# Kernel optimization log

Measured on AMD Instinct MI355X. Metric: run time of the kernel, lower is better.

The kernel has to match this reference:

```python
import jax, jax.numpy as jnp
import numpy as np

N_ANCHORS = 10647
N_CLASSES = 80
N_OUT = 5 + N_CLASSES
N_GT = 2048
POS_IOU = 0.7
NEG_IOU = 0.3
N_SAMPLE = 256
POS_RATIO = 0.5


def _cxcy_to_corners(b):
    return jnp.concatenate([b[:, :2] - b[:, 2:4] / 2, b[:, :2] + b[:, 2:4] / 2], axis=-1)


def _iou(a, b):
    # a: [N,4] corner boxes, b: [M,4] corner boxes -> [N,M]
    lt = jnp.maximum(a[:, None, :2], b[None, :, :2])
    rb = jnp.minimum(a[:, None, 2:], b[None, :, 2:])
    wh = jnp.clip(rb - lt, 0.0)
    inter = wh[..., 0] * wh[..., 1]
    area_a = (a[:, 2] - a[:, 0]) * (a[:, 3] - a[:, 1])
    area_b = (b[:, 2] - b[:, 0]) * (b[:, 3] - b[:, 1])
    return inter / (area_a[:, None] + area_b[None, :] - inter)


def _bce_logits(x, t):
    # numerically stable BCEWithLogits, elementwise
    return jnp.maximum(x, 0.0) - x * t + jnp.log1p(jnp.exp(-jnp.abs(x)))


def _demote_first(labels, value, excess):
    # demote the first `excess` anchors (in index order) whose label == value to -1,
    # mirroring torch's nonzero()[randperm(excess)] which always hits the first
    # `excess` entries of the nonzero list
    m = labels == value
    cum = jnp.cumsum(m.astype(jnp.int32))
    return jnp.where(m & (cum <= excess), -1.0, labels)


def _generate_targets(priors, gt_boxes, gt_labels):
    ious = _iou(_cxcy_to_corners(priors[:, :4]), _cxcy_to_corners(gt_boxes))  # [N, M]
    gt_max_index = jnp.argmax(ious, axis=0)       # [M] best anchor per gt
    anchor_max_ious = jnp.max(ious, axis=1)       # [N]
    anchor_max_index = jnp.argmax(ious, axis=1)   # [N]
    labels = jnp.full((N_ANCHORS,), -1.0, dtype=ious.dtype)
    labels = labels.at[gt_max_index].set(1.0)
    labels = jnp.where(anchor_max_ious >= POS_IOU, 1.0, labels)
    labels = jnp.where(anchor_max_ious < NEG_IOU, 0.0, labels)
    n_pos_quota = int(POS_RATIO * N_SAMPLE)
    n_pos_actual = jnp.sum(labels == 1.0)
    labels = _demote_first(labels, 1.0, jnp.maximum(n_pos_actual - n_pos_quota, 0))
    n_neg_req = N_SAMPLE - jnp.sum(labels == 1.0)
    n_neg_actual = jnp.sum(labels == 0.0)
    labels = _demote_first(labels, 0.0, jnp.maximum(n_neg_actual - n_neg_req, 0))
    anchor_gt_box = gt_boxes[anchor_max_index]    # [N,4] matched gt box per anchor
    anchor_cls = gt_labels[anchor_max_index] + 5  # [N] one-hot class column per anchor
    targets = jnp.zeros((N_ANCHORS, N_OUT), dtype=gt_boxes.dtype)
    targets = targets.at[:, :4].set(anchor_gt_box)
    targets = targets.at[:, 4].set(labels)
    targets = targets.at[jnp.arange(N_ANCHORS), anchor_cls].set(1.0)
    return targets


def _forward(predictions, gt_boxes, gt_labels, priors):
    targets = _generate_targets(priors, gt_boxes, gt_labels)
    pred = predictions[0]                          # [N, N_OUT]
    labels = targets[:, 4]
    pos = (labels == 1.0).astype(pred.dtype)
    neg = (labels == 0.0).astype(pred.dtype)
    n_pos = jnp.maximum(jnp.sum(pos), 1.0)
    n_neg = jnp.maximum(jnp.sum(neg), 1.0)
    # masked-mean MSE over x,y,w,h on positive anchors
    diff2 = (pred[:, :4] - targets[:, :4]) ** 2
    loss_box = jnp.sum(pos[:, None] * diff2, axis=0) / n_pos
    loss_conf_obj = jnp.sum(pos * _bce_logits(pred[:, 4], targets[:, 4])) / n_pos
    loss_conf_nonobj = jnp.sum(neg * _bce_logits(pred[:, 4], targets[:, 4])) / n_neg
    loss_class = jnp.sum(pos[:, None] * _bce_logits(pred[:, 5:], targets[:, 5:])) / (n_pos * N_CLASSES)
    total_loss = jnp.sum(loss_box) + loss_conf_obj + loss_conf_nonobj + loss_class
    return pred, total_loss


def setup_inputs() -> dict:
    key = jax.random.key(0)
    k1, k2, k3, k4 = jax.random.split(key, 4)
    predictions = jax.random.normal(k1, (1, N_ANCHORS, N_OUT), dtype=jnp.float32)
    gt_boxes = jax.random.uniform(k2, (N_GT, 4), dtype=jnp.float32, minval=0.05, maxval=0.95)
    gt_labels = jax.random.randint(k3, (N_GT,), 0, N_CLASSES)
    priors = jax.random.uniform(k4, (N_ANCHORS, N_OUT), dtype=jnp.float32, minval=0.05, maxval=0.95)
    return {"predictions": predictions, "gt_boxes": gt_boxes, "gt_labels": gt_labels, "priors": priors}


def reference(predictions, gt_boxes, gt_labels, priors):
    return _forward(predictions, gt_boxes, gt_labels, priors)
```

## Files before the change

### kernel.cpp

```cpp
#include <hip/hip_runtime.h>
#include <math.h>

#define N_ANCH 10647
#define N_GT   2048
#define N_OUTC 85
#define PRED_ELEMS (N_ANCH * N_OUTC)
#define PRED_V4    (PRED_ELEMS / 4)
#define N_CHUNK    42
#define NBLK_A     176
#define NBLK_G     336
#define NBLK_IOU   (NBLK_A + NBLK_G)
#define CPY_PER_BLK ((PRED_V4 + NBLK_IOU - 1) / NBLK_IOU)

struct WS {
    unsigned long long akey[N_ANCH];
    unsigned long long gkey[N_GT];
    int lab[N_ANCH];
    int cnt_p[N_CHUNK], cnt_n[N_CHUNK];
    float acc[3];
};

__device__ __forceinline__ float bce(float x, float t) {
    return fmaxf(x, 0.0f) - x * t + log1pf(expf(-fabsf(x)));
}

__device__ __forceinline__ unsigned long long packkey(float iou, int idx) {
    return ((unsigned long long)__float_as_uint(iou) << 32) |
           (unsigned)(~(unsigned)idx);
}

__device__ __forceinline__ float iou_one(const float4& a, float aa,
                                         const float4& g, float ga) {
    float lx = fmaxf(a.x, g.x), ly = fmaxf(a.y, g.y);
    float rx = fminf(a.z, g.z), ry = fminf(a.w, g.w);
    float w  = fmaxf(rx - lx, 0.0f), h = fmaxf(ry - ly, 0.0f);
    float inter = w * h;
    return inter / ((aa + ga) - inter);
}

__global__ __launch_bounds__(256) void k_iou(const float* __restrict__ pred,
                                             const float* __restrict__ gtb,
                                             const float* __restrict__ priors,
                                             float* __restrict__ out,
                                             WS* __restrict__ ws) {
    int b = blockIdx.x, t = threadIdx.x;
    for (int k = t; k < CPY_PER_BLK; k += 256) {
        int idx = b * CPY_PER_BLK + k;
        if (idx < PRED_V4)
            ((float4*)out)[idx] = ((const float4*)pred)[idx];
    }
    if (b == 0 && t == 0) {
        out[PRED_ELEMS - 3] = pred[PRED_ELEMS - 3];
        out[PRED_ELEMS - 2] = pred[PRED_ELEMS - 2];
        out[PRED_ELEMS - 1] = pred[PRED_ELEMS - 1];
    }

    __shared__ float4 sc[128];
    __shared__ float  sa[128];

    if (b < NBLK_A) {
        int bx = b % 11, by = b / 11;
        int jbase = by * 128;
        if (t < 128) {
            float4 v = ((const float4*)gtb)[jbase + t];
            float4 c = make_float4(v.x - v.z*0.5f, v.y - v.w*0.5f,
                                   v.x + v.z*0.5f, v.y + v.w*0.5f);
            sc[t] = c;
            sa[t] = (c.z - c.x) * (c.w - c.y);
        }
        float4 a[4]; float aa[4]; int iarr[4]; bool val[4];
#pragma unroll
        for (int u = 0; u < 4; ++u) {
            int i = bx * 1024 + u * 256 + t;
            iarr[u] = i; val[u] = (i < N_ANCH);
            a[u] = make_float4(0.f, 0.f, 0.f, 0.f); aa[u] = 0.f;
            if (val[u]) {
                float cx = priors[i*N_OUTC+0], cy = priors[i*N_OUTC+1];
                float w  = priors[i*N_OUTC+2], h  = priors[i*N_OUTC+3];
                a[u] = make_float4(cx - w*0.5f, cy - h*0.5f, cx + w*0.5f, cy + h*0.5f);
                aa[u] = (a[u].z - a[u].x) * (a[u].w - a[u].y);
            }
        }
        __syncthreads();
        float bi[4] = {-1.f, -1.f, -1.f, -1.f};
        int bj[4] = {0, 0, 0, 0};
#pragma unroll 2
        for (int jj = 0; jj < 128; ++jj) {
            float4 g = sc[jj]; float ga = sa[jj];
#pragma unroll
            for (int u = 0; u < 4; ++u) {
                float iou = iou_one(a[u], aa[u], g, ga);
                bool c = iou > bi[u];
                bi[u] = c ? iou : bi[u];
                bj[u] = c ? jj : bj[u];
            }
        }
#pragma unroll
        for (int u = 0; u < 4; ++u)
            if (val[u]) atomicMax(&ws->akey[iarr[u]], packkey(bi[u], jbase + bj[u]));
    } else {
        int b2 = b - NBLK_A;
        int bx = b2 % 4, by = b2 / 4;
        int ibase = by * 128;
        if (t < 128) {
            int i = ibase + t;
            float4 c = make_float4(0.f, 0.f, 0.f, 0.f);
            float ar = 0.f;
            if (i < N_ANCH) {
                float cx = priors[i*N_OUTC+0], cy = priors[i*N_OUTC+1];
                float w  = priors[i*N_OUTC+2], h  = priors[i*N_OUTC+3];
                c = make_float4(cx - w*0.5f, cy - h*0.5f, cx + w*0.5f, cy + h*0.5f);
                ar = (c.z - c.x) * (c.w - c.y);
            }
            sc[t] = c; sa[t] = ar;
        }
        int j0 = bx * 512 + t, j1 = j0 + 256;
        float4 v = ((const float4*)gtb)[j0];
        float4 g0 = make_float4(v.x - v.z*0.5f, v.y - v.w*0.5f,
                                v.x + v.z*0.5f, v.y + v.w*0.5f);
        float ga0 = (g0.z - g0.x) * (g0.w - g0.y);
        v = ((const float4*)gtb)[j1];
        float4 g1 = make_float4(v.x - v.z*0.5f, v.y - v.w*0.5f,
                                v.x + v.z*0.5f, v.y + v.w*0.5f);
        float ga1 = (g1.z - g1.x) * (g1.w - g1.y);
        __syncthreads();
        float bi0 = -1.0f, bi1 = -1.0f;
        int bii0 = 0, bii1 = 0;
#pragma unroll 4
        for (int ii = 0; ii < 128; ++ii) {
            float4 ax = sc[ii]; float aax = sa[ii];
            float iou0 = iou_one(ax, aax, g0, ga0);
            float iou1 = iou_one(ax, aax, g1, ga1);
            bool c0 = iou0 > bi0;
            bi0 = c0 ? iou0 : bi0; bii0 = c0 ? ii : bii0;
            bool c1 = iou1 > bi1;
            bi1 = c1 ? iou1 : bi1; bii1 = c1 ? ii : bii1;
        }
        atomicMax(&ws->gkey[j0], packkey(bi0, ibase + bii0));
        atomicMax(&ws->gkey[j1], packkey(bi1, ibase + bii1));
    }
}

__global__ __launch_bounds__(256) void k_label(WS* __restrict__ ws) {
    __shared__ int flg[256];
    __shared__ int wp[4], wn[4];
    int b = blockIdx.x, t = threadIdx.x, base = b * 256;
    int lane = t & 63, wid = t >> 6;
    flg[t] = 0;
    __syncthreads();
    for (int j = t; j < N_GT; j += 256) {
        int ai = (int)(~(unsigned)(ws->gkey[j]));
        int rel = ai - base;
        if ((unsigned)rel < 256u) flg[rel] = 1;
    }
    __syncthreads();
    int i = base + t;
    int lab = -2;
    if (i < N_ANCH) {
        float amax = __uint_as_float((unsigned)(ws->akey[i] >> 32));
        lab = (amax < 0.3f) ? 0 : ((amax >= 0.7f || flg[t]) ? 1 : -1);
        ws->lab[i] = lab;
    }
    unsigned long long b1 = __ballot(lab == 1), b0 = __ballot(lab == 0);
    if (lane == 0) { wp[wid] = __popcll(b1); wn[wid] = __popcll(b0); }
    __syncthreads();
    if (t == 0) {
        ws->cnt_p[b] = wp[0] + wp[1] + wp[2] + wp[3];
        ws->cnt_n[b] = wn[0] + wn[1] + wn[2] + wn[3];
    }
}

__global__ __launch_bounds__(256) void k_closs(const float* __restrict__ pred,
                                               const float* __restrict__ gtb,
                                               const int* __restrict__ gtl,
                                               WS* __restrict__ ws) {
    __shared__ int wps[4], wns[4];
    __shared__ int    sPosI[256];
    __shared__ float4 sPosBox[256];
    __shared__ int    sPosCls[256];
    __shared__ int    sNegI[256];
    __shared__ float  red[12];
    int b = blockIdx.x, t = threadIdx.x, lane = t & 63, wid = t >> 6;

    int npa = 0, nna = 0, pb = 0, nb = 0;
#pragma unroll
    for (int c = 0; c < N_CHUNK; ++c) {
        int cp = ws->cnt_p[c], cn = ws->cnt_n[c];
        if (c < b) { pb += cp; nb += cn; }
        npa += cp; nna += cn;
    }
    int excess_pos = (npa > 128) ? (npa - 128) : 0;
    int n_pos_f = npa - excess_pos;
    int n_neg_req = 256 - n_pos_f;
    int excess_neg = (nna > n_neg_req) ? (nna - n_neg_req) : 0;

    int i = b * 256 + t;
    int lab = (i < N_ANCH) ? ws->lab[i] : -2;
    bool f1 = (lab == 1), f0 = (lab == 0);
    unsigned long long b1 = __ballot(f1), b0v = __ballot(f0);
    unsigned long long pm = (2ull << lane) - 1ull;
    int r1 = __popcll(b1 & pm), r0 = __popcll(b0v & pm);
    if (lane == 0) { wps[wid] = __popcll(b1); wns[wid] = __popcll(b0v); }
    __syncthreads();
    int p1 = 0, p0 = 0, cpB = 0, cnB = 0;
    for (int w = 0; w < 4; ++w) {
        int v1 = wps[w], v0 = wns[w];
        cpB += v1; cnB += v0;
        if (w < wid) { p1 += v1; p0 += v0; }
    }
    int thp = excess_pos - pb; thp = (thp < 0) ? 0 : thp;
    int thn = excess_neg - nb; thn = (thn < 0) ? 0 : thn;
    if (f1) {
        int L = p1 + r1;
        if (L > thp) {
            int slot = L - thp - 1;
            sPosI[slot] = i;
            unsigned am = ~(unsigned)(ws->akey[i]);
            sPosBox[slot] = ((const float4*)gtb)[am];
            sPosCls[slot] = gtl[am] + 5;
        }
    }
    if (f0) {
        int L = p0 + r0;
        if (L > thn) sNegI[L - thn - 1] = i;
    }
    __syncthreads();
    int nP = cpB - thp; nP = (nP < 0) ? 0 : nP;
    int nN = cnB - thn; nN = (nN < 0) ? 0 : nN;

    float acc_a = 0.f, acc_c = 0.f, acc_n = 0.f;
    int nT = nP * N_OUTC;
    for (int u = t; u < nT; u += 256) {
        int pi = u / N_OUTC, col = u - pi * N_OUTC;
        float p = pred[sPosI[pi] * N_OUTC + col];
        if (col < 4) {
            float d = p - ((const float*)&sPosBox[pi])[col];
            acc_a += d * d;
        } else if (col == 4) {
            acc_a += bce(p, 1.0f);
        } else {
            acc_c += bce(p, (col == sPosCls[pi]) ? 1.0f : 0.0f);
        }
    }
    for (int u = t; u < nN; u += 256)
        acc_n += bce(pred[sNegI[u] * N_OUTC + 4], 0.0f);

    for (int o = 32; o; o >>= 1) {
        acc_a += __shfl_down(acc_a, o);
        acc_c += __shfl_down(acc_c, o);
        acc_n += __shfl_down(acc_n, o);
    }
    if (lane == 0) { red[wid] = acc_a; red[4 + wid] = acc_c; red[8 + wid] = acc_n; }
    __syncthreads();
    if (t == 0) {
        float A  = red[0] + red[1] + red[2]  + red[3];
        float C  = red[4] + red[5] + red[6]  + red[7];
        float Nn = red[8] + red[9] + red[10] + red[11];
        if (A  != 0.f) atomicAdd(&ws->acc[0], A);
        if (C  != 0.f) atomicAdd(&ws->acc[1], C);
        if (Nn != 0.f) atomicAdd(&ws->acc[2], Nn);
    }
}

__global__ __launch_bounds__(64) void k_final(WS* __restrict__ ws,
                                              float* __restrict__ out) {
    int t = threadIdx.x;
    int cp = (t < N_CHUNK) ? ws->cnt_p[t] : 0;
    int cn = (t < N_CHUNK) ? ws->cnt_n[t] : 0;
    for (int o = 32; o; o >>= 1) { cp += __shfl_down(cp, o); cn += __shfl_down(cn, o); }
    if (t == 0) {
        int npa = cp, nna = cn;
        int excess_pos = (npa > 128) ? (npa - 128) : 0;
        int n_pos_f = npa - excess_pos;
        int n_neg_req = 256 - n_pos_f;
        int excess_neg = (nna > n_neg_req) ? (nna - n_neg_req) : 0;
        int n_neg_f = nna - excess_neg;
        float np = fmaxf((float)n_pos_f, 1.0f);
        float nn = fmaxf((float)n_neg_f, 1.0f);
        out[PRED_ELEMS] = ws->acc[0] / np + ws->acc[2] / nn + ws->acc[1] / (np * 80.0f);
    }
}

extern "C" void kernel_launch(void* const* d_in, const int* in_sizes, int n_in,
                              void* d_out, int out_size, void* d_ws, size_t ws_size,
                              hipStream_t stream) {
    const float* pred   = (const float*)d_in[0];
    const float* gtb    = (const float*)d_in[1];
    const int*   gtl    = (const int*)d_in[2];
    const float* priors = (const float*)d_in[3];
    float* out = (float*)d_out;
    WS* ws = (WS*)d_ws;

    hipMemsetAsync(d_ws, 0, sizeof(WS), stream);
    k_iou<<<dim3(NBLK_IOU), 256, 0, stream>>>(pred, gtb, priors, out, ws);
    k_label<<<dim3(N_CHUNK), 256, 0, stream>>>(ws);
    k_closs<<<dim3(N_CHUNK), 256, 0, stream>>>(pred, gtb, gtl, ws);
    k_final<<<1, 64, 0, stream>>>(ws, out);
}
```

Before: 77.60 us.

## Defer IoU division via cross-multiplied compare and retile IoU blocks smaller

The argmax loops now track intersection and area sum and compare candidates by cross-multiplication, so the per-pair division is replaced by a single division per thread at the end. Tiles shrink from 128 to 64 boxes and anchors per thread drop from 4 to 2, which raises the block count (672 plus 668) for better occupancy and load balance. The workspace is reordered so the memset clears only the atomic keys and accumulators instead of the whole struct. The cross-multiplied compare could break ties or rounding edge cases differently from the direct IoU comparison, and there are more atomics because each anchor or GT is now covered by more tiles.

```diff
diff --git a/kernel.cpp b/kernel.cpp
--- a/kernel.cpp
+++ b/kernel.cpp
@@ -7,18 +7,25 @@
 #define PRED_ELEMS (N_ANCH * N_OUTC)
 #define PRED_V4    (PRED_ELEMS / 4)
 #define N_CHUNK    42
-#define NBLK_A     176
-#define NBLK_G     336
-#define NBLK_IOU   (NBLK_A + NBLK_G)
+
+#define ABX 21
+#define ABY 32
+#define NBLK_A (ABX * ABY)
+#define GBX 4
+#define GBY 167
+#define NBLK_G (GBX * GBY)
+#define NBLK_IOU (NBLK_A + NBLK_G)
 #define CPY_PER_BLK ((PRED_V4 + NBLK_IOU - 1) / NBLK_IOU)
 
 struct WS {
     unsigned long long akey[N_ANCH];
     unsigned long long gkey[N_GT];
+    float acc[3];
+    float pad_;
     int lab[N_ANCH];
     int cnt_p[N_CHUNK], cnt_n[N_CHUNK];
-    float acc[3];
 };
+#define MEMSET_BYTES (N_ANCH * 8 + N_GT * 8 + 16)
 
 __device__ __forceinline__ float bce(float x, float t) {
     return fmaxf(x, 0.0f) - x * t + log1pf(expf(-fabsf(x)));
@@ -27,15 +34,6 @@
 __device__ __forceinline__ unsigned long long packkey(float iou, int idx) {
     return ((unsigned long long)__float_as_uint(iou) << 32) |
            (unsigned)(~(unsigned)idx);
-}
-
-__device__ __forceinline__ float iou_one(const float4& a, float aa,
-                                         const float4& g, float ga) {
-    float lx = fmaxf(a.x, g.x), ly = fmaxf(a.y, g.y);
-    float rx = fminf(a.z, g.z), ry = fminf(a.w, g.w);
-    float w  = fmaxf(rx - lx, 0.0f), h = fmaxf(ry - ly, 0.0f);
-    float inter = w * h;
-    return inter / ((aa + ga) - inter);
 }
 
 __global__ __launch_bounds__(256) void k_iou(const float* __restrict__ pred,
@@ -44,8 +42,8 @@
                                              float* __restrict__ out,
                                              WS* __restrict__ ws) {
     int b = blockIdx.x, t = threadIdx.x;
-    for (int k = t; k < CPY_PER_BLK; k += 256) {
-        int idx = b * CPY_PER_BLK + k;
+    if (t < CPY_PER_BLK) {
+        int idx = b * CPY_PER_BLK + t;
         if (idx < PRED_V4)
             ((float4*)out)[idx] = ((const float4*)pred)[idx];
     }
@@ -55,54 +53,61 @@
         out[PRED_ELEMS - 1] = pred[PRED_ELEMS - 1];
     }
 
-    __shared__ float4 sc[128];
-    __shared__ float  sa[128];
+    __shared__ float4 sc[64];
+    __shared__ float  sa[64];
 
     if (b < NBLK_A) {
-        int bx = b % 11, by = b / 11;
-        int jbase = by * 128;
-        if (t < 128) {
+        int bx = b % ABX, by = b / ABX;
+        int jbase = by * 64;
+        if (t < 64) {
             float4 v = ((const float4*)gtb)[jbase + t];
             float4 c = make_float4(v.x - v.z*0.5f, v.y - v.w*0.5f,
                                    v.x + v.z*0.5f, v.y + v.w*0.5f);
             sc[t] = c;
             sa[t] = (c.z - c.x) * (c.w - c.y);
         }
-        float4 a[4]; float aa[4]; int iarr[4]; bool val[4];
-#pragma unroll
-        for (int u = 0; u < 4; ++u) {
-            int i = bx * 1024 + u * 256 + t;
-            iarr[u] = i; val[u] = (i < N_ANCH);
-            a[u] = make_float4(0.f, 0.f, 0.f, 0.f); aa[u] = 0.f;
-            if (val[u]) {
-                float cx = priors[i*N_OUTC+0], cy = priors[i*N_OUTC+1];
-                float w  = priors[i*N_OUTC+2], h  = priors[i*N_OUTC+3];
-                a[u] = make_float4(cx - w*0.5f, cy - h*0.5f, cx + w*0.5f, cy + h*0.5f);
-                aa[u] = (a[u].z - a[u].x) * (a[u].w - a[u].y);
-            }
+        int i0 = bx * 512 + t, i1 = i0 + 256;
+        bool v0 = (i0 < N_ANCH), v1 = (i1 < N_ANCH);
+        float4 a0 = make_float4(0.f,0.f,0.f,0.f), a1 = a0;
+        float aa0 = 0.f, aa1 = 0.f;
+        if (v0) {
+            float cx = priors[i0*N_OUTC+0], cy = priors[i0*N_OUTC+1];
+            float w  = priors[i0*N_OUTC+2], h  = priors[i0*N_OUTC+3];
+            a0 = make_float4(cx - w*0.5f, cy - h*0.5f, cx + w*0.5f, cy + h*0.5f);
+            aa0 = (a0.z - a0.x) * (a0.w - a0.y);
+        }
+        if (v1) {
+            float cx = priors[i1*N_OUTC+0], cy = priors[i1*N_OUTC+1];
+            float w  = priors[i1*N_OUTC+2], h  = priors[i1*N_OUTC+3];
+            a1 = make_float4(cx - w*0.5f, cy - h*0.5f, cx + w*0.5f, cy + h*0.5f);
+            aa1 = (a1.z - a1.x) * (a1.w - a1.y);
         }
         __syncthreads();
-        float bi[4] = {-1.f, -1.f, -1.f, -1.f};
-        int bj[4] = {0, 0, 0, 0};
-#pragma unroll 2
-        for (int jj = 0; jj < 128; ++jj) {
+        float I0 = -1.f, S0 = 1.f, I1 = -1.f, S1 = 1.f;
+        int bj0 = 0, bj1 = 0;
+#pragma unroll 4
+        for (int jj = 0; jj < 64; ++jj) {
             float4 g = sc[jj]; float ga = sa[jj];
-#pragma unroll
-            for (int u = 0; u < 4; ++u) {
-                float iou = iou_one(a[u], aa[u], g, ga);
-                bool c = iou > bi[u];
-                bi[u] = c ? iou : bi[u];
-                bj[u] = c ? jj : bj[u];
-            }
-        }
-#pragma unroll
-        for (int u = 0; u < 4; ++u)
-            if (val[u]) atomicMax(&ws->akey[iarr[u]], packkey(bi[u], jbase + bj[u]));
+            float lx = fmaxf(a0.x, g.x), ly = fmaxf(a0.y, g.y);
+            float rx = fminf(a0.z, g.z), ry = fminf(a0.w, g.w);
+            float In = fmaxf(rx - lx, 0.f) * fmaxf(ry - ly, 0.f);
+            float Sn = aa0 + ga;
+            bool c = In * S0 > I0 * Sn;
+            I0 = c ? In : I0; S0 = c ? Sn : S0; bj0 = c ? jj : bj0;
+            lx = fmaxf(a1.x, g.x); ly = fmaxf(a1.y, g.y);
+            rx = fminf(a1.z, g.z); ry = fminf(a1.w, g.w);
+            In = fmaxf(rx - lx, 0.f) * fmaxf(ry - ly, 0.f);
+            Sn = aa1 + ga;
+            c = In * S1 > I1 * Sn;
+            I1 = c ? In : I1; S1 = c ? Sn : S1; bj1 = c ? jj : bj1;
+        }
+        if (v0) atomicMax(&ws->akey[i0], packkey(I0 / (S0 - I0), jbase + bj0));
+        if (v1) atomicMax(&ws->akey[i1], packkey(I1 / (S1 - I1), jbase + bj1));
     } else {
         int b2 = b - NBLK_A;
-        int bx = b2 % 4, by = b2 / 4;
-        int ibase = by * 128;
-        if (t < 128) {
+        int bx = b2 % GBX, by = b2 / GBX;
+        int ibase = by * 64;
+        if (t < 64) {
             int i = ibase + t;
             float4 c = make_float4(0.f, 0.f, 0.f, 0.f);
             float ar = 0.f;
@@ -124,20 +129,26 @@
                                 v.x + v.z*0.5f, v.y + v.w*0.5f);
         float ga1 = (g1.z - g1.x) * (g1.w - g1.y);
         __syncthreads();
-        float bi0 = -1.0f, bi1 = -1.0f;
-        int bii0 = 0, bii1 = 0;
+        float I0 = -1.f, S0 = 1.f, I1 = -1.f, S1 = 1.f;
+        int bi0 = 0, bi1 = 0;
 #pragma unroll 4
-        for (int ii = 0; ii < 128; ++ii) {
-            float4 ax = sc[ii]; float aax = sa[ii];
-            float iou0 = iou_one(ax, aax, g0, ga0);
-            float iou1 = iou_one(ax, aax, g1, ga1);
-            bool c0 = iou0 > bi0;
-            bi0 = c0 ? iou0 : bi0; bii0 = c0 ? ii : bii0;
-            bool c1 = iou1 > bi1;
-            bi1 = c1 ? iou1 : bi1; bii1 = c1 ? ii : bii1;
-        }
-        atomicMax(&ws->gkey[j0], packkey(bi0, ibase + bii0));
-        atomicMax(&ws->gkey[j1], packkey(bi1, ibase + bii1));
+        for (int ii = 0; ii < 64; ++ii) {
+            float4 a = sc[ii]; float aa = sa[ii];
+            float lx = fmaxf(a.x, g0.x), ly = fmaxf(a.y, g0.y);
+            float rx = fminf(a.z, g0.z), ry = fminf(a.w, g0.w);
+            float In = fmaxf(rx - lx, 0.f) * fmaxf(ry - ly, 0.f);
+            float Sn = aa + ga0;
+            bool c = In * S0 > I0 * Sn;
+            I0 = c ? In : I0; S0 = c ? Sn : S0; bi0 = c ? ii : bi0;
+            lx = fmaxf(a.x, g1.x); ly = fmaxf(a.y, g1.y);
+            rx = fminf(a.z, g1.z); ry = fminf(a.w, g1.w);
+            In = fmaxf(rx - lx, 0.f) * fmaxf(ry - ly, 0.f);
+            Sn = aa + ga1;
+            c = In * S1 > I1 * Sn;
+            I1 = c ? In : I1; S1 = c ? Sn : S1; bi1 = c ? ii : bi1;
+        }
+        atomicMax(&ws->gkey[j0], packkey(I0 / (S0 - I0), ibase + bi0));
+        atomicMax(&ws->gkey[j1], packkey(I1 / (S1 - I1), ibase + bi1));
     }
 }
 
@@ -291,7 +302,7 @@
     float* out = (float*)d_out;
     WS* ws = (WS*)d_ws;
 
-    hipMemsetAsync(d_ws, 0, sizeof(WS), stream);
+    hipMemsetAsync(d_ws, 0, MEMSET_BYTES, stream);
     k_iou<<<dim3(NBLK_IOU), 256, 0, stream>>>(pred, gtb, priors, out, ws);
     k_label<<<dim3(N_CHUNK), 256, 0, stream>>>(ws);
     k_closs<<<dim3(N_CHUNK), 256, 0, stream>>>(pred, gtb, gtl, ws);
```

Measured after the change: 69.55 us. 10.4% less time.
